# Optimization experiments

Measured on AMD Instinct MI355X. Metric: run time of the kernel, lower is better.

## Reference

```python
import jax, jax.numpy as jnp
import numpy as np

B, N, D = 16, 2048, 1024
H, DH = 8, 64
I = H * DH            # 512
L = 64                # num_latents
DEPTH = 6
FF = 4 * D


def setup_inputs() -> dict:
    key = jax.random.key(0)
    ks = jax.random.split(key, 8)
    s = 0.02  # weight scale to keep activations well-conditioned
    return {
        "x": jax.random.normal(ks[0], (B, N, D), jnp.float32),
        "mask": jax.random.randint(ks[1], (B, N), 0, 2, jnp.int32),
        "latents": jax.random.normal(ks[2], (L, D), jnp.float32),
        "ln_m_w": jnp.ones((DEPTH, D), jnp.float32),
        "ln_m_b": jnp.zeros((DEPTH, D), jnp.float32),
        "ln_l_w": jnp.ones((DEPTH, D), jnp.float32),
        "ln_l_b": jnp.zeros((DEPTH, D), jnp.float32),
        "Wq": jax.random.normal(ks[3], (DEPTH, D, I), jnp.float32) * s,
        "Wkv": jax.random.normal(ks[4], (DEPTH, D, 2 * I), jnp.float32) * s,
        "Wo": jax.random.normal(ks[5], (DEPTH, I, D), jnp.float32) * s,
        "ff_ln_w": jnp.ones((DEPTH, D), jnp.float32),
        "ff_ln_b": jnp.zeros((DEPTH, D), jnp.float32),
        "W1": jax.random.normal(ks[6], (DEPTH, D, FF), jnp.float32) * s,
        "W2": jax.random.normal(ks[7], (DEPTH, FF, D), jnp.float32) * s,
        "norm_w": jnp.ones((D,), jnp.float32),
        "norm_b": jnp.zeros((D,), jnp.float32),
    }


def _ln(x, w, b, eps=1e-5):
    mu = x.mean(-1, keepdims=True)
    var = ((x - mu) ** 2).mean(-1, keepdims=True)
    return (x - mu) * jax.lax.rsqrt(var + eps) * w + b


def reference(x, mask, latents, ln_m_w, ln_m_b, ln_l_w, ln_l_b,
              Wq, Wkv, Wo, ff_ln_w, ff_ln_b, W1, W2, norm_w, norm_b):
    b, n, d = x.shape
    Lq = latents.shape[0]
    depth = Wq.shape[0]
    h = H
    dh = Wq.shape[-1] // h
    scale = dh ** -0.5

    x4 = x[:, None]  # b 1 n d  (t = 1 media frame)
    lat = jnp.broadcast_to(latents, (b, 1, Lq, d)).astype(x.dtype)
    # mask==1 means masked-out; latents (L zeros) are always attendable
    fmask = jnp.concatenate([mask, jnp.zeros((b, Lq), mask.dtype)], axis=-1)
    mbool = (fmask == 1)[:, None, None, None, :]  # b 1 1 1 S -> broadcast to b t h i S

    for i in range(depth):
        xn = _ln(x4, ln_m_w[i], ln_m_b[i])
        lnl = _ln(lat, ln_l_w[i], ln_l_b[i])
        q = (lnl @ Wq[i]).reshape(b, 1, Lq, h, dh)
        kv = jnp.concatenate([xn, lnl], axis=-2) @ Wkv[i]  # b 1 S 2I
        k, v = jnp.split(kv, 2, axis=-1)
        S = k.shape[-2]
        k = k.reshape(b, 1, S, h, dh)
        v = v.reshape(b, 1, S, h, dh)
        sim = jnp.einsum('btihd,btjhd->bthij', q, k) * scale
        sim = jnp.where(mbool, -jnp.inf, sim)
        sim = sim - jax.lax.stop_gradient(sim.max(axis=-1, keepdims=True))
        attn = jax.nn.softmax(sim, axis=-1)
        out = jnp.einsum('bthij,btjhd->btihd', attn, v).reshape(b, 1, Lq, h * dh)
        lat = out @ Wo[i] + lat
        hf = jax.nn.gelu(_ln(lat, ff_ln_w[i], ff_ln_b[i]) @ W1[i], approximate=False)
        lat = hf @ W2[i] + lat
    return _ln(lat, norm_w, norm_b)
```

## Files before the change

### kernel.cpp

```cpp
#include <hip/hip_runtime.h>

typedef unsigned short u16;
typedef unsigned int u32;
typedef __attribute__((ext_vector_type(8))) short short8;
typedef __attribute__((ext_vector_type(4))) float f4;

#define DEV static __device__ __forceinline__

constexpr int BB = 16, NN = 2048, DD = 1024, HH = 8, DHD = 64, II = 512, LL = 64, DEPTHC = 6, FFC = 4096;

DEV u16 f2bf(float f) {
  union { float f; u32 u; } v; v.f = f;
  u32 r = v.u + 0x7FFFu + ((v.u >> 16) & 1u);
  return (u16)(r >> 16);
}

typedef const u32 __attribute__((address_space(1)))* gas_p;
typedef u32 __attribute__((address_space(3)))* las_p;
DEV void gl_lds16(const void* g, void* l) {
  __builtin_amdgcn_global_load_lds((gas_p)g, (las_p)l, 16, 0, 0);
}

__global__ __launch_bounds__(256) void maskscan_k(const int* __restrict__ mask,
    int* __restrict__ idx, int* __restrict__ cnt) {
  int b = blockIdx.x, tid = threadIdx.x;
  int lane = tid & 63, wv = tid >> 6;
  const int* mrow = mask + (size_t)b * NN;
  int base = tid * 8;
  int keep[8]; int local = 0;
  #pragma unroll
  for (int j = 0; j < 8; j++) { keep[j] = (mrow[base + j] == 0); local += keep[j]; }
  int incl = local;
  #pragma unroll
  for (int off = 1; off < 64; off <<= 1) {
    int v = __shfl_up(incl, off, 64);
    if (lane >= off) incl += v;
  }
  __shared__ int wsum[4];
  if (lane == 63) wsum[wv] = incl;
  __syncthreads();
  int wbase = 0;
  for (int w = 0; w < wv; w++) wbase += wsum[w];
  int pos = wbase + incl - local;
  #pragma unroll
  for (int j = 0; j < 8; j++) if (keep[j]) idx[(size_t)b * NN + pos++] = base + j;
  if (tid == 255) cnt[b] = wbase + incl;
}

__global__ __launch_bounds__(256) void ln_gather_k(const float* __restrict__ x,
    const int* __restrict__ idx, const int* __restrict__ cnt, u16* __restrict__ xcomp) {
  int b = blockIdx.y, j = blockIdx.x, tid = threadIdx.x;
  int c = cnt[b];
  if (j >= ((c + 127) & ~127)) return;
  ushort4* orow = (ushort4*)(xcomp + ((size_t)b * NN + j) * DD);
  if (j >= c) { orow[tid] = make_ushort4(0, 0, 0, 0); return; }
  int src = idx[(size_t)b * NN + j];
  const float4* rp = (const float4*)(x + ((size_t)b * NN + src) * DD);
  float4 v = rp[tid];
  float s = v.x + v.y + v.z + v.w;
  float s2 = v.x*v.x + v.y*v.y + v.z*v.z + v.w*v.w;
  #pragma unroll
  for (int off = 32; off >= 1; off >>= 1) {
    s  += __shfl_xor(s, off, 64);
    s2 += __shfl_xor(s2, off, 64);
  }
  __shared__ float red[8];
  int wv = tid >> 6;
  if ((tid & 63) == 0) { red[wv] = s; red[4 + wv] = s2; }
  __syncthreads();
  s  = red[0] + red[1] + red[2] + red[3];
  s2 = red[4] + red[5] + red[6] + red[7];
  float mu = s * (1.f / DD);
  float var = s2 * (1.f / DD) - mu * mu;
  float rstd = rsqrtf(var + 1e-5f);
  orow[tid] = make_ushort4(f2bf((v.x - mu) * rstd), f2bf((v.y - mu) * rstd),
                           f2bf((v.z - mu) * rstd), f2bf((v.w - mu) * rstd));
}

template<bool OUTF32>
__global__ __launch_bounds__(256) void ln_rows_k(const float* __restrict__ in,
    const float* __restrict__ w, const float* __restrict__ bias, void* __restrict__ out) {
  int row = blockIdx.x;
  int tid = threadIdx.x;
  const float4* rp = (const float4*)(in + (size_t)row * DD);
  float4 x = rp[tid];
  float s = x.x + x.y + x.z + x.w;
  float s2 = x.x*x.x + x.y*x.y + x.z*x.z + x.w*x.w;
  #pragma unroll
  for (int off = 32; off >= 1; off >>= 1) {
    s  += __shfl_xor(s, off, 64);
    s2 += __shfl_xor(s2, off, 64);
  }
  __shared__ float red[8];
  int wv = tid >> 6;
  if ((tid & 63) == 0) { red[wv] = s; red[4 + wv] = s2; }
  __syncthreads();
  s  = red[0] + red[1] + red[2] + red[3];
  s2 = red[4] + red[5] + red[6] + red[7];
  float mu = s * (1.f / DD);
  float var = s2 * (1.f / DD) - mu * mu;
  float rstd = rsqrtf(var + 1e-5f);
  float y[4] = {x.x, x.y, x.z, x.w};
  int col = tid * 4;
  #pragma unroll
  for (int j = 0; j < 4; j++)
    y[j] = (y[j] - mu) * rstd * w[col + j] + bias[col + j];
  if (OUTF32) {
    float4 o = {y[0], y[1], y[2], y[3]};
    ((float4*)out)[(size_t)row * (DD/4) + tid] = o;
  } else {
    ushort4 o = make_ushort4(f2bf(y[0]), f2bf(y[1]), f2bf(y[2]), f2bf(y[3]));
    ((ushort4*)out)[(size_t)row * (DD/4) + tid] = o;
  }
}

__global__ __launch_bounds__(256) void lat_init_k(const float* __restrict__ latents, float* __restrict__ lat) {
  int idx = blockIdx.x * 256 + threadIdx.x;
  ((float4*)lat)[idx] = ((const float4*)latents)[idx & (LL * DD / 4 - 1)];
}

__global__ void zero_k(float* __restrict__ p, int n) {
  int i = blockIdx.x * 256 + threadIdx.x;
  if (i < n) p[i] = 0.f;
}

__global__ void transpall_k(const float* __restrict__ WqA, const float* __restrict__ WkvA,
    const float* __restrict__ WoA, const float* __restrict__ W1A, const float* __restrict__ W2A,
    const float* __restrict__ lnwA, const float* __restrict__ lnbA,
    u16* __restrict__ WqkvTA, u16* __restrict__ WkvTfA, u16* __restrict__ WoTA,
    u16* __restrict__ W1TA, u16* __restrict__ W2TA, float* __restrict__ biaskvA) {
  __shared__ float t[32][33];
  __shared__ float bred[8][32];
  int gid = blockIdx.x;
  int depth = gid / 10240;
  int id = gid % 10240;
  const float* in; u16* o1; int R, C, c0, r0;
  bool iskv = false;
  if (id < 512)       { in = WqA  + (size_t)depth*1024*512;  R = 1024; C = 512;  int l = id;        c0 = (l % 16) * 32;  r0 = (l / 16) * 32;  o1 = WqkvTA + (size_t)depth*1536*1024; }
  else if (id < 1536) { in = WkvA + (size_t)depth*1024*1024; R = 1024; C = 1024; int l = id - 512;  c0 = (l % 32) * 32;  r0 = (l / 32) * 32;  o1 = WqkvTA + (size_t)depth*1536*1024 + 512*1024; iskv = true; }
  else if (id < 2048) { in = WoA  + (size_t)depth*512*1024;  R = 512;  C = 1024; int l = id - 1536; c0 = (l % 32) * 32;  r0 = (l / 32) * 32;  o1 = WoTA + (size_t)depth*1024*512; }
  else if (id < 6144) { in = W1A  + (size_t)depth*1024*4096; R = 1024; C = 4096; int l = id - 2048; c0 = (l % 128) * 32; r0 = (l / 128) * 32; o1 = W1TA + (size_t)depth*4096*1024; }
  else                { in = W2A  + (size_t)depth*4096*1024; R = 4096; C = 1024; int l = id - 6144; c0 = (l % 32) * 32;  r0 = (l / 32) * 32;  o1 = W2TA + (size_t)depth*1024*4096; }
  int tx = threadIdx.x, ty = threadIdx.y;
  #pragma unroll
  for (int j = 0; j < 4; j++)
    t[ty + j*8][tx] = in[(size_t)(r0 + ty + j*8) * C + c0 + tx];
  __syncthreads();
  #pragma unroll
  for (int j = 0; j < 4; j++)
    o1[(size_t)(c0 + ty + j*8) * R + r0 + tx] = f2bf(t[tx][ty + j*8]);
  if (iskv) {
    const float* lnw = lnwA + depth * 1024;
    const float* lnb = lnbA + depth * 1024;
    u16* WkvTf = WkvTfA + (size_t)depth*1024*1024;
    float sc = lnw[r0 + tx];
    #pragma unroll
    for (int j = 0; j < 4; j++)
      WkvTf[(size_t)(c0 + ty + j*8) * 1024 + r0 + tx] = f2bf(t[tx][ty + j*8] * sc);
    float partial = 0.f;
    #pragma unroll
    for (int rr = 0; rr < 4; rr++)
      partial += lnb[r0 + ty + rr*8] * t[ty + rr*8][tx];
    bred[ty][tx] = partial;
    __syncthreads();
    if (ty == 0) {
      float sum = 0.f;
      #pragma unroll
      for (int w = 0; w < 8; w++) sum += bred[w][tx];
      atomicAdd(&biaskvA[depth*1024 + c0 + tx], sum);
    }
  }
}

__global__ __launch_bounds__(256) void gemm_fused_k(
    const u16* __restrict__ xcomp, const u16* __restrict__ WkvTf, u16* __restrict__ kvx,
    const float* __restrict__ bias, const int* __restrict__ cnt,
    const u16* __restrict__ lnl, const u16* __restrict__ WqkvT, u16* __restrict__ qkv) {
  __shared__ __align__(16) u16 As[128 * 32];
  __shared__ __align__(16) u16 Bs[128 * 32];
  int id = blockIdx.x;
  int tid = threadIdx.x;
  int wv = tid >> 6, lane = tid & 63;
  const u16 *A, *B; u16* C; int N; bool dobias;
  int m0, n0;
  if (id < 2048) {
    int xg = id & 7, t = id >> 3;
    int mtile = xg * 32 + (t >> 3);
    n0 = (t & 7) * 128;
    int batch = mtile >> 4;
    int ml = (mtile & 15) * 128;
    if (ml >= cnt[batch]) return;
    m0 = batch * NN + ml;
    A = xcomp; B = WkvTf; C = kvx; N = 1024; dobias = true;
  } else {
    int l = id - 2048;
    m0 = (l / 12) * 128; n0 = (l % 12) * 128;
    A = lnl; B = WqkvT; C = qkv; N = 1536; dobias = false;
  }
  const int K = 1024;
  int srow = wv * 16 + (lane >> 2);
  int scol = (lane & 3) * 8;
  const u16* gA0 = A + (size_t)(m0 + srow) * K + scol;
  const u16* gA1 = A + (size_t)(m0 + 64 + srow) * K + scol;
  const u16* gB0 = B + (size_t)(n0 + srow) * K + scol;
  const u16* gB1 = B + (size_t)(n0 + 64 + srow) * K + scol;
  u16* lA0 = &As[srow * 32 + scol];
  u16* lA1 = &As[(64 + srow) * 32 + scol];
  u16* lB0 = &Bs[srow * 32 + scol];
  u16* lB1 = &Bs[(64 + srow) * 32 + scol];
  int wm = (wv & 1) * 64, wn = (wv >> 1) * 64;
  int fr = lane & 15, fq = (lane >> 4) * 8;
  f4 acc[4][4];
  #pragma unroll
  for (int mi = 0; mi < 4; mi++)
    #pragma unroll
    for (int ni = 0; ni < 4; ni++) acc[mi][ni] = f4{0.f, 0.f, 0.f, 0.f};

  for (int k0 = 0; k0 < K; k0 += 32) {
    gl_lds16(gA0 + k0, lA0);
    gl_lds16(gA1 + k0, lA1);
    gl_lds16(gB0 + k0, lB0);
    gl_lds16(gB1 + k0, lB1);
    __syncthreads();
    short8 af[4], bfr[4];
    #pragma unroll
    for (int mi = 0; mi < 4; mi++)
      af[mi] = *(const short8*)&As[(wm + mi*16 + fr) * 32 + fq];
    #pragma unroll
    for (int ni = 0; ni < 4; ni++)
      bfr[ni] = *(const short8*)&Bs[(wn + ni*16 + fr) * 32 + fq];
    #pragma unroll
    for (int mi = 0; mi < 4; mi++)
      #pragma unroll
      for (int ni = 0; ni < 4; ni++)
        acc[mi][ni] = __builtin_amdgcn_mfma_f32_16x16x32_bf16(af[mi], bfr[ni], acc[mi][ni], 0, 0, 0);
    __syncthreads();
  }
  int er = (lane >> 4) * 4;
  int ec = lane & 15;
  #pragma unroll
  for (int mi = 0; mi < 4; mi++) {
    #pragma unroll
    for (int ni = 0; ni < 4; ni++) {
      int col = n0 + wn + ni*16 + ec;
      float bv = dobias ? bias[col] : 0.f;
      #pragma unroll
      for (int r = 0; r < 4; r++) {
        int row = m0 + wm + mi*16 + er + r;
        C[(size_t)row * N + col] = f2bf(acc[mi][ni][r] + bv);
      }
    }
  }
}

__global__ __launch_bounds__(256) void gemm_gelu_k(const u16* __restrict__ A, const u16* __restrict__ Bm,
    u16* __restrict__ C, int M, int N, int K) {
  __shared__ __align__(16) u16 As[128 * 32];
  __shared__ __align__(16) u16 Bs[128 * 32];
  int tid = threadIdx.x;
  int wv = tid >> 6, lane = tid & 63;
  int m0 = blockIdx.y * 128, n0 = blockIdx.x * 128;
  int srow = wv * 16 + (lane >> 2);
  int scol = (lane & 3) * 8;
  const u16* gA0 = A + (size_t)(m0 + srow) * K + scol;
  const u16* gA1 = A + (size_t)(m0 + 64 + srow) * K + scol;
  const u16* gB0 = Bm + (size_t)(n0 + srow) * K + scol;
  const u16* gB1 = Bm + (size_t)(n0 + 64 + srow) * K + scol;
  u16* lA0 = &As[srow * 32 + scol];
  u16* lA1 = &As[(64 + srow) * 32 + scol];
  u16* lB0 = &Bs[srow * 32 + scol];
  u16* lB1 = &Bs[(64 + srow) * 32 + scol];
  int wm = (wv & 1) * 64, wn = (wv >> 1) * 64;
  int fr = lane & 15, fq = (lane >> 4) * 8;
  f4 acc[4][4];
  #pragma unroll
  for (int mi = 0; mi < 4; mi++)
    #pragma unroll
    for (int ni = 0; ni < 4; ni++) acc[mi][ni] = f4{0.f, 0.f, 0.f, 0.f};

  for (int k0 = 0; k0 < K; k0 += 32) {
    gl_lds16(gA0 + k0, lA0);
    gl_lds16(gA1 + k0, lA1);
    gl_lds16(gB0 + k0, lB0);
    gl_lds16(gB1 + k0, lB1);
    __syncthreads();
    short8 af[4], bfr[4];
    #pragma unroll
    for (int mi = 0; mi < 4; mi++)
      af[mi] = *(const short8*)&As[(wm + mi*16 + fr) * 32 + fq];
    #pragma unroll
    for (int ni = 0; ni < 4; ni++)
      bfr[ni] = *(const short8*)&Bs[(wn + ni*16 + fr) * 32 + fq];
    #pragma unroll
    for (int mi = 0; mi < 4; mi++)
      #pragma unroll
      for (int ni = 0; ni < 4; ni++)
        acc[mi][ni] = __builtin_amdgcn_mfma_f32_16x16x32_bf16(af[mi], bfr[ni], acc[mi][ni], 0, 0, 0);
    __syncthreads();
  }
  int er = (lane >> 4) * 4;
  int ec = lane & 15;
  #pragma unroll
  for (int mi = 0; mi < 4; mi++)
    #pragma unroll
    for (int ni = 0; ni < 4; ni++) {
      int col = n0 + wn + ni*16 + ec;
      #pragma unroll
      for (int r = 0; r < 4; r++) {
        int row = m0 + wm + mi*16 + er + r;
        float v = acc[mi][ni][r];
        v = 0.5f * v * (1.f + erff(v * 0.70710678118654752f));
        C[(size_t)row * N + col] = f2bf(v);
      }
    }
}

__global__ __launch_bounds__(256) void gemmsk_k(const u16* __restrict__ A, const u16* __restrict__ Bm,
    float* __restrict__ C, int M, int N, int K, int Kc) {
  __shared__ __align__(16) u16 As[128 * 32];
  __shared__ __align__(16) u16 Bs[128 * 32];
  int tid = threadIdx.x;
  int wv = tid >> 6, lane = tid & 63;
  int m0 = blockIdx.y * 128, n0 = blockIdx.x * 128;
  int kb = blockIdx.z * Kc;
  int srow = wv * 16 + (lane >> 2);
  int scol = (lane & 3) * 8;
  const u16* gA0 = A + (size_t)(m0 + srow) * K + kb + scol;
  const u16* gA1 = A + (size_t)(m0 + 64 + srow) * K + kb + scol;
  const u16* gB0 = Bm + (size_t)(n0 + srow) * K + kb + scol;
  const u16* gB1 = Bm + (size_t)(n0 + 64 + srow) * K + kb + scol;
  u16* lA0 = &As[srow * 32 + scol];
  u16* lA1 = &As[(64 + srow) * 32 + scol];
  u16* lB0 = &Bs[srow * 32 + scol];
  u16* lB1 = &Bs[(64 + srow) * 32 + scol];
  int wm = (wv & 1) * 64, wn = (wv >> 1) * 64;
  int fr = lane & 15, fq = (lane >> 4) * 8;
  f4 acc[4][4];
  #pragma unroll
  for (int mi = 0; mi < 4; mi++)
    #pragma unroll
    for (int ni = 0; ni < 4; ni++) acc[mi][ni] = f4{0.f, 0.f, 0.f, 0.f};

  for (int k0 = 0; k0 < Kc; k0 += 32) {
    gl_lds16(gA0 + k0, lA0);
    gl_lds16(gA1 + k0, lA1);
    gl_lds16(gB0 + k0, lB0);
    gl_lds16(gB1 + k0, lB1);
    __syncthreads();
    short8 af[4], bfr[4];
    #pragma unroll
    for (int mi = 0; mi < 4; mi++)
      af[mi] = *(const short8*)&As[(wm + mi*16 + fr) * 32 + fq];
    #pragma unroll
    for (int ni = 0; ni < 4; ni++)
      bfr[ni] = *(const short8*)&Bs[(wn + ni*16 + fr) * 32 + fq];
    #pragma unroll
    for (int mi = 0; mi < 4; mi++)
      #pragma unroll
      for (int ni = 0; ni < 4; ni++)
        acc[mi][ni] = __builtin_amdgcn_mfma_f32_16x16x32_bf16(af[mi], bfr[ni], acc[mi][ni], 0, 0, 0);
    __syncthreads();
  }
  int er = (lane >> 4) * 4;
  int ec = lane & 15;
  #pragma unroll
  for (int mi = 0; mi < 4; mi++)
    #pragma unroll
    for (int ni = 0; ni < 4; ni++) {
      int col = n0 + wn + ni*16 + ec;
      #pragma unroll
      for (int r = 0; r < 4; r++) {
        int row = m0 + wm + mi*16 + er + r;
        atomicAdd(&C[(size_t)row * N + col], acc[mi][ni][r]);
      }
    }
}

__global__ __launch_bounds__(256) void attn_part_k(const u16* __restrict__ qkv,
    const u16* __restrict__ kvx, const int* __restrict__ cnt,
    float* __restrict__ opart, float* __restrict__ mlpart) {
  int id = blockIdx.x;
  int b = id >> 4;
  int h = (id >> 1) & 7;
  int half = id & 1;
  int tid = threadIdx.x;
  int wv = tid >> 6, lane = tid & 63;
  int fr = lane & 15, fq8 = (lane >> 4) * 8;
  int c = cnt[b];
  int nt = (c + 63) >> 6;
  int T = nt + 1;
  int t0 = half ? (T >> 1) : 0;
  int t1 = half ? T : (T >> 1);

  __shared__ __align__(16) u16 ks[64 * 88];
  __shared__ __align__(16) u16 vs[64 * 88];
  __shared__ __align__(16) u16 ps[4][16 * 88];
  __shared__ float smask[64];

  const u16* qp = qkv + (size_t)(b * LL + wv * 16 + fr) * 1536 + h * DHD;
  short8 aq0 = *(const short8*)(qp + fq8);
  short8 aq1 = *(const short8*)(qp + 32 + fq8);

  float m_i[4], l_i[4];
  f4 o[4];
  #pragma unroll
  for (int r = 0; r < 4; r++) { m_i[r] = -1e30f; l_i[r] = 0.f; }
  #pragma unroll
  for (int dt = 0; dt < 4; dt++) o[dt] = f4{0.f, 0.f, 0.f, 0.f};

  const float scale = 0.125f;

  for (int t = t0; t < t1; t++) {
    bool isLat = (t == nt);
    const u16* src;
    int rs;
    if (isLat) { src = qkv + (size_t)(b * LL) * 1536 + 512 + h * DHD; rs = 1536; }
    else       { src = kvx + (size_t)(b * NN + t * 64) * 1024 + h * DHD; rs = 1024; }
    __syncthreads();
    #pragma unroll
    for (int it = 0; it < 2; it++) {
      int cid = it * 256 + tid;
      int kr = cid >> 3, c8 = (cid & 7) * 8;
      int4 kvv = *(const int4*)(src + (size_t)kr * rs + c8);
      *(int4*)&ks[kr * 88 + c8] = kvv;
      int4 vvv = *(const int4*)(src + 512 + (size_t)kr * rs + c8);
      const u16* ve = (const u16*)&vvv;
      #pragma unroll
      for (int j = 0; j < 8; j++) vs[(c8 + j) * 88 + kr] = ve[j];
    }
    if (tid < 64)
      smask[tid] = (isLat || (t * 64 + tid < c)) ? 0.f : -1e30f;
    __syncthreads();

    f4 sim[4];
    #pragma unroll
    for (int ct = 0; ct < 4; ct++) {
      short8 b0 = *(const short8*)&ks[(ct*16 + fr) * 88 + fq8];
      short8 b1 = *(const short8*)&ks[(ct*16 + fr) * 88 + 32 + fq8];
      f4 s = f4{0.f, 0.f, 0.f, 0.f};
      s = __builtin_amdgcn_mfma_f32_16x16x32_bf16(aq0, b0, s, 0, 0, 0);
      s = __builtin_amdgcn_mfma_f32_16x16x32_bf16(aq1, b1, s, 0, 0, 0);
      float mk = smask[ct*16 + fr];
      #pragma unroll
      for (int r = 0; r < 4; r++) s[r] = s[r] * scale + mk;
      sim[ct] = s;
    }
    float mnew[4], alpha[4], p[4][4];
    #pragma unroll
    for (int r = 0; r < 4; r++) {
      float mx = fmaxf(fmaxf(sim[0][r], sim[1][r]), fmaxf(sim[2][r], sim[3][r]));
      #pragma unroll
      for (int off = 8; off >= 1; off >>= 1) mx = fmaxf(mx, __shfl_xor(mx, off, 16));
      mnew[r] = fmaxf(m_i[r], mx);
      alpha[r] = __expf(m_i[r] - mnew[r]);
      m_i[r] = mnew[r];
      float ssum = 0.f;
      #pragma unroll
      for (int ct = 0; ct < 4; ct++) { float e = __expf(sim[ct][r] - mnew[r]); p[ct][r] = e; ssum += e; }
      #pragma unroll
      for (int off = 8; off >= 1; off >>= 1) ssum += __shfl_xor(ssum, off, 16);
      l_i[r] = l_i[r] * alpha[r] + ssum;
    }
    #pragma unroll
    for (int ct = 0; ct < 4; ct++)
      #pragma unroll
      for (int r = 0; r < 4; r++)
        ps[wv][((lane>>4)*4 + r) * 88 + ct*16 + fr] = f2bf(p[ct][r]);
    #pragma unroll
    for (int dt = 0; dt < 4; dt++)
      #pragma unroll
      for (int r = 0; r < 4; r++) o[dt][r] *= alpha[r];
    short8 pa0 = *(const short8*)&ps[wv][fr * 88 + fq8];
    short8 pa1 = *(const short8*)&ps[wv][fr * 88 + 32 + fq8];
    #pragma unroll
    for (int dt = 0; dt < 4; dt++) {
      short8 bv0 = *(const short8*)&vs[(dt*16 + fr) * 88 + fq8];
      short8 bv1 = *(const short8*)&vs[(dt*16 + fr) * 88 + 32 + fq8];
      o[dt] = __builtin_amdgcn_mfma_f32_16x16x32_bf16(pa0, bv0, o[dt], 0, 0, 0);
      o[dt] = __builtin_amdgcn_mfma_f32_16x16x32_bf16(pa1, bv1, o[dt], 0, 0, 0);
    }
  }
  #pragma unroll
  for (int dt = 0; dt < 4; dt++)
    #pragma unroll
    for (int r = 0; r < 4; r++) {
      int row = wv * 16 + (lane>>4)*4 + r;
      int col = dt*16 + fr;
      opart[((size_t)id * 64 + row) * 64 + col] = o[dt][r];
    }
  if (fr == 0) {
    #pragma unroll
    for (int r = 0; r < 4; r++) {
      int row = wv * 16 + (lane>>4)*4 + r;
      mlpart[id * 128 + row * 2]     = m_i[r];
      mlpart[id * 128 + row * 2 + 1] = l_i[r];
    }
  }
}

__global__ __launch_bounds__(256) void attn_comb_k(const float* __restrict__ opart,
    const float* __restrict__ mlpart, u16* __restrict__ out) {
  int bh = blockIdx.x;
  int b = bh >> 3, h = bh & 7;
  int id0 = bh * 2, id1 = bh * 2 + 1;
  int tid = threadIdx.x;
  int row = tid >> 2;
  int c0 = (tid & 3) * 16;
  float m0 = mlpart[id0 * 128 + row * 2], l0 = mlpart[id0 * 128 + row * 2 + 1];
  float m1 = mlpart[id1 * 128 + row * 2], l1 = mlpart[id1 * 128 + row * 2 + 1];
  float m = fmaxf(m0, m1);
  float a0 = __expf(m0 - m), a1 = __expf(m1 - m);
  float rl = 1.f / (l0 * a0 + l1 * a1);
  const float4* p0 = (const float4*)(opart + ((size_t)id0 * 64 + row) * 64 + c0);
  const float4* p1 = (const float4*)(opart + ((size_t)id1 * 64 + row) * 64 + c0);
  u16* op = out + ((size_t)(b * LL + row)) * II + h * DHD + c0;
  #pragma unroll
  for (int j = 0; j < 4; j++) {
    float4 v0 = p0[j], v1 = p1[j];
    op[j*4 + 0] = f2bf((v0.x * a0 + v1.x * a1) * rl);
    op[j*4 + 1] = f2bf((v0.y * a0 + v1.y * a1) * rl);
    op[j*4 + 2] = f2bf((v0.z * a0 + v1.z * a1) * rl);
    op[j*4 + 3] = f2bf((v0.w * a0 + v1.w * a1) * rl);
  }
}

extern "C" void kernel_launch(void* const* d_in, const int* in_sizes, int n_in,
                              void* d_out, int out_size, void* d_ws, size_t ws_size,
                              hipStream_t stream) {
  (void)in_sizes; (void)n_in; (void)out_size; (void)ws_size;
  const float* x       = (const float*)d_in[0];
  const int*   mask    = (const int*)d_in[1];
  const float* latents = (const float*)d_in[2];
  const float* ln_m_w  = (const float*)d_in[3];
  const float* ln_m_b  = (const float*)d_in[4];
  const float* ln_l_w  = (const float*)d_in[5];
  const float* ln_l_b  = (const float*)d_in[6];
  const float* Wq      = (const float*)d_in[7];
  const float* Wkv     = (const float*)d_in[8];
  const float* Wo      = (const float*)d_in[9];
  const float* ff_ln_w = (const float*)d_in[10];
  const float* ff_ln_b = (const float*)d_in[11];
  const float* W1      = (const float*)d_in[12];
  const float* W2      = (const float*)d_in[13];
  const float* norm_w  = (const float*)d_in[14];
  const float* norm_b  = (const float*)d_in[15];
  float* out = (float*)d_out;

  char* ws = (char*)d_ws;
  size_t off = 0;
  auto alloc = [&](size_t bytes) -> void* {
    void* p = ws + off; off += (bytes + 255) & ~(size_t)255; return p;
  };
  u16* xcomp = (u16*)alloc((size_t)32768 * 1024 * 2);
  u16* kvx   = (u16*)alloc((size_t)32768 * 1024 * 2);
  int* idxb  = (int*)alloc((size_t)32768 * 4);
  int* cnt   = (int*)alloc(64);
  float* lat = (float*)alloc((size_t)1024 * 1024 * 4);
  u16* lnl   = (u16*)alloc((size_t)1024 * 1024 * 2);
  u16* latn  = (u16*)alloc((size_t)1024 * 1024 * 2);
  u16* qkv   = (u16*)alloc((size_t)1024 * 1536 * 2);
  u16* aout  = (u16*)alloc((size_t)1024 * 512 * 2);
  u16* hf    = (u16*)alloc((size_t)1024 * 4096 * 2);
  float* opart  = (float*)alloc((size_t)256 * 64 * 64 * 4);
  float* mlpart = (float*)alloc((size_t)256 * 128 * 4);
  u16* WqkvT = (u16*)alloc((size_t)DEPTHC * 1536 * 1024 * 2);
  u16* WkvTf = (u16*)alloc((size_t)DEPTHC * 1024 * 1024 * 2);
  u16* WoT   = (u16*)alloc((size_t)DEPTHC * 1024 * 512 * 2);
  u16* W1T   = (u16*)alloc((size_t)DEPTHC * 4096 * 1024 * 2);
  u16* W2T   = (u16*)alloc((size_t)DEPTHC * 1024 * 4096 * 2);
  float* biaskv_all = (float*)alloc(DEPTHC * 1024 * 4);

  maskscan_k<<<16, 256, 0, stream>>>(mask, idxb, cnt);
  ln_gather_k<<<dim3(2048, 16), 256, 0, stream>>>(x, idxb, cnt, xcomp);
  lat_init_k<<<1024, 256, 0, stream>>>(latents, lat);
  zero_k<<<24, 256, 0, stream>>>(biaskv_all, DEPTHC * 1024);
  transpall_k<<<DEPTHC * 10240, dim3(32, 8), 0, stream>>>(
      Wq, Wkv, Wo, W1, W2, ln_m_w, ln_m_b,
      WqkvT, WkvTf, WoT, W1T, W2T, biaskv_all);

  for (int i = 0; i < DEPTHC; i++) {
    ln_rows_k<false><<<1024, 256, 0, stream>>>(lat, ln_l_w + i*1024, ln_l_b + i*1024, lnl);
    gemm_fused_k<<<2144, 256, 0, stream>>>(
        xcomp, WkvTf + (size_t)i*1024*1024, kvx, biaskv_all + i*1024, cnt,
        lnl, WqkvT + (size_t)i*1536*1024, qkv);
    attn_part_k<<<256, 256, 0, stream>>>(qkv, kvx, cnt, opart, mlpart);
    attn_comb_k<<<128, 256, 0, stream>>>(opart, mlpart, aout);
    gemmsk_k<<<dim3(8, 8, 4), 256, 0, stream>>>(aout, WoT + (size_t)i*1024*512, lat, 1024, 1024, 512, 128);
    ln_rows_k<false><<<1024, 256, 0, stream>>>(lat, ff_ln_w + i*1024, ff_ln_b + i*1024, latn);
    gemm_gelu_k<<<dim3(32, 8), 256, 0, stream>>>(latn, W1T + (size_t)i*4096*1024, hf, 1024, 4096, 1024);
    gemmsk_k<<<dim3(8, 8, 4), 256, 0, stream>>>(hf, W2T + (size_t)i*1024*4096, lat, 1024, 1024, 4096, 1024);
  }
  ln_rows_k<true><<<1024, 256, 0, stream>>>(lat, norm_w, norm_b, out);
}
```

Baseline: 1.497 ms.

## Fuse layernorms into GEMMs, merge setup kernels, transpose V layout

Folds the latent and feed-forward layernorm affine parameters into pre-transposed weights plus precomputed bias vectors. The per-row normalization now runs inside the QKV and W1 GEMM prologues, so the separate ln_rows launches go away. The attention-combine step is merged into the Wo GEMM, and the small setup kernels are merged into one launch. The transpose kernel moves to 64x64 tiles with 16-byte packed stores, and K/V are written split with V transposed, so the attention kernel no longer scatters V into LDS. The cost is more work per GEMM block: redundant row statistics and a float-to-bf16 conversion on the A-tile path.

```diff
diff --git a/kernel.cpp b/kernel.cpp
--- a/kernel.cpp
+++ b/kernel.cpp
@@ -15,36 +15,54 @@
   return (u16)(r >> 16);
 }
 
+DEV void pack8(const float* v, u16* dst) {
+  union { u16 u[8]; int4 i; } p;
+  #pragma unroll
+  for (int e = 0; e < 8; e++) p.u[e] = f2bf(v[e]);
+  *(int4*)dst = p.i;
+}
+
 typedef const u32 __attribute__((address_space(1)))* gas_p;
 typedef u32 __attribute__((address_space(3)))* las_p;
 DEV void gl_lds16(const void* g, void* l) {
   __builtin_amdgcn_global_load_lds((gas_p)g, (las_p)l, 16, 0, 0);
 }
 
-__global__ __launch_bounds__(256) void maskscan_k(const int* __restrict__ mask,
-    int* __restrict__ idx, int* __restrict__ cnt) {
-  int b = blockIdx.x, tid = threadIdx.x;
-  int lane = tid & 63, wv = tid >> 6;
-  const int* mrow = mask + (size_t)b * NN;
-  int base = tid * 8;
-  int keep[8]; int local = 0;
-  #pragma unroll
-  for (int j = 0; j < 8; j++) { keep[j] = (mrow[base + j] == 0); local += keep[j]; }
-  int incl = local;
-  #pragma unroll
-  for (int off = 1; off < 64; off <<= 1) {
-    int v = __shfl_up(incl, off, 64);
-    if (lane >= off) incl += v;
-  }
-  __shared__ int wsum[4];
-  if (lane == 63) wsum[wv] = incl;
-  __syncthreads();
-  int wbase = 0;
-  for (int w = 0; w < wv; w++) wbase += wsum[w];
-  int pos = wbase + incl - local;
-  #pragma unroll
-  for (int j = 0; j < 8; j++) if (keep[j]) idx[(size_t)b * NN + pos++] = base + j;
-  if (tid == 255) cnt[b] = wbase + incl;
+__global__ __launch_bounds__(256) void pre0_k(const int* __restrict__ mask,
+    int* __restrict__ idx, int* __restrict__ cnt,
+    const float* __restrict__ latents, float* __restrict__ lat,
+    float* __restrict__ biasall, int nbias) {
+  int bid = blockIdx.x, tid = threadIdx.x;
+  if (bid < 16) {
+    int b = bid;
+    int lane = tid & 63, wv = tid >> 6;
+    const int* mrow = mask + (size_t)b * NN;
+    int base = tid * 8;
+    int keep[8]; int local = 0;
+    #pragma unroll
+    for (int j = 0; j < 8; j++) { keep[j] = (mrow[base + j] == 0); local += keep[j]; }
+    int incl = local;
+    #pragma unroll
+    for (int off = 1; off < 64; off <<= 1) {
+      int v = __shfl_up(incl, off, 64);
+      if (lane >= off) incl += v;
+    }
+    __shared__ int wsum[4];
+    if (lane == 63) wsum[wv] = incl;
+    __syncthreads();
+    int wbase = 0;
+    for (int w = 0; w < wv; w++) wbase += wsum[w];
+    int pos = wbase + incl - local;
+    #pragma unroll
+    for (int j = 0; j < 8; j++) if (keep[j]) idx[(size_t)b * NN + pos++] = base + j;
+    if (tid == 255) cnt[b] = wbase + incl;
+  } else if (bid < 16 + 1024) {
+    int i = (bid - 16) * 256 + tid;
+    ((float4*)lat)[i] = ((const float4*)latents)[i & (LL * DD / 4 - 1)];
+  } else {
+    int i = ((bid - 1040) * 256 + tid) * 4;
+    if (i < nbias) *(float4*)(biasall + i) = float4{0.f, 0.f, 0.f, 0.f};
+  }
 }
 
 __global__ __launch_bounds__(256) void ln_gather_k(const float* __restrict__ x,
@@ -77,9 +95,8 @@
                            f2bf((v.z - mu) * rstd), f2bf((v.w - mu) * rstd));
 }
 
-template<bool OUTF32>
-__global__ __launch_bounds__(256) void ln_rows_k(const float* __restrict__ in,
-    const float* __restrict__ w, const float* __restrict__ bias, void* __restrict__ out) {
+__global__ __launch_bounds__(256) void ln_final_k(const float* __restrict__ in,
+    const float* __restrict__ w, const float* __restrict__ bias, float* __restrict__ out) {
   int row = blockIdx.x;
   int tid = threadIdx.x;
   const float4* rp = (const float4*)(in + (size_t)row * DD);
@@ -100,112 +117,423 @@
   float mu = s * (1.f / DD);
   float var = s2 * (1.f / DD) - mu * mu;
   float rstd = rsqrtf(var + 1e-5f);
-  float y[4] = {x.x, x.y, x.z, x.w};
   int col = tid * 4;
-  #pragma unroll
-  for (int j = 0; j < 4; j++)
-    y[j] = (y[j] - mu) * rstd * w[col + j] + bias[col + j];
-  if (OUTF32) {
-    float4 o = {y[0], y[1], y[2], y[3]};
-    ((float4*)out)[(size_t)row * (DD/4) + tid] = o;
+  float4 o;
+  o.x = (x.x - mu) * rstd * w[col+0] + bias[col+0];
+  o.y = (x.y - mu) * rstd * w[col+1] + bias[col+1];
+  o.z = (x.z - mu) * rstd * w[col+2] + bias[col+2];
+  o.w = (x.w - mu) * rstd * w[col+3] + bias[col+3];
+  ((float4*)out)[(size_t)row * (DD/4) + tid] = o;
+}
+
+__global__ __launch_bounds__(256) void transpall_k(const float* __restrict__ WqA,
+    const float* __restrict__ WkvA, const float* __restrict__ WoA,
+    const float* __restrict__ W1A, const float* __restrict__ W2A,
+    const float* __restrict__ lnlw, const float* __restrict__ lnlb,
+    const float* __restrict__ lnmw, const float* __restrict__ lnmb,
+    const float* __restrict__ ffw, const float* __restrict__ ffb,
+    u16* __restrict__ WqkvTA, u16* __restrict__ WkvTfA, u16* __restrict__ WoTA,
+    u16* __restrict__ W1TA, u16* __restrict__ W2TA, float* __restrict__ biasall) {
+  __shared__ float t[64][67];
+  __shared__ float sw1[64], sw2[64], sb1[64], sb2[64];
+  __shared__ float bred[64][4];
+  int gid = blockIdx.x, tid = threadIdx.x;
+  int depth = gid / 2560;
+  int id = gid % 2560;
+  float* biasqkv = biasall + depth * 1536;
+  float* biaskv  = biasall + DEPTHC*1536 + depth * 1024;
+  float* bias1   = biasall + DEPTHC*1536 + DEPTHC*1024 + depth * 4096;
+  const float* in; int R, C, c0, r0;
+  u16 *o1, *o2 = nullptr;
+  const float *w1v = nullptr, *w2v = nullptr, *b1v = nullptr, *b2v = nullptr;
+  float *bo1 = nullptr, *bo2 = nullptr;
+  if (id < 128) {
+    in = WqA + (size_t)depth*1024*512; R = 1024; C = 512;
+    r0 = (id >> 3) * 64; c0 = (id & 7) * 64;
+    o1 = WqkvTA + (size_t)depth*1536*1024;
+    w1v = lnlw + depth*1024; b1v = lnlb + depth*1024; bo1 = biasqkv;
+  } else if (id < 384) {
+    int l = id - 128;
+    in = WkvA + (size_t)depth*1024*1024; R = 1024; C = 1024;
+    r0 = (l >> 4) * 64; c0 = (l & 15) * 64;
+    o1 = WqkvTA + (size_t)depth*1536*1024 + (size_t)512*1024;
+    w1v = lnlw + depth*1024; b1v = lnlb + depth*1024; bo1 = biasqkv + 512;
+    o2 = WkvTfA + (size_t)depth*1024*1024;
+    w2v = lnmw + depth*1024; b2v = lnmb + depth*1024; bo2 = biaskv;
+  } else if (id < 512) {
+    int l = id - 384;
+    in = WoA + (size_t)depth*512*1024; R = 512; C = 1024;
+    r0 = (l >> 4) * 64; c0 = (l & 15) * 64;
+    o1 = WoTA + (size_t)depth*1024*512;
+  } else if (id < 1536) {
+    int l = id - 512;
+    in = W1A + (size_t)depth*1024*4096; R = 1024; C = 4096;
+    r0 = (l >> 6) * 64; c0 = (l & 63) * 64;
+    o1 = W1TA + (size_t)depth*4096*1024;
+    w1v = ffw + depth*1024; b1v = ffb + depth*1024; bo1 = bias1;
   } else {
-    ushort4 o = make_ushort4(f2bf(y[0]), f2bf(y[1]), f2bf(y[2]), f2bf(y[3]));
-    ((ushort4*)out)[(size_t)row * (DD/4) + tid] = o;
-  }
-}
-
-__global__ __launch_bounds__(256) void lat_init_k(const float* __restrict__ latents, float* __restrict__ lat) {
-  int idx = blockIdx.x * 256 + threadIdx.x;
-  ((float4*)lat)[idx] = ((const float4*)latents)[idx & (LL * DD / 4 - 1)];
-}
-
-__global__ void zero_k(float* __restrict__ p, int n) {
-  int i = blockIdx.x * 256 + threadIdx.x;
-  if (i < n) p[i] = 0.f;
-}
-
-__global__ void transpall_k(const float* __restrict__ WqA, const float* __restrict__ WkvA,
-    const float* __restrict__ WoA, const float* __restrict__ W1A, const float* __restrict__ W2A,
-    const float* __restrict__ lnwA, const float* __restrict__ lnbA,
-    u16* __restrict__ WqkvTA, u16* __restrict__ WkvTfA, u16* __restrict__ WoTA,
-    u16* __restrict__ W1TA, u16* __restrict__ W2TA, float* __restrict__ biaskvA) {
-  __shared__ float t[32][33];
-  __shared__ float bred[8][32];
-  int gid = blockIdx.x;
-  int depth = gid / 10240;
-  int id = gid % 10240;
-  const float* in; u16* o1; int R, C, c0, r0;
-  bool iskv = false;
-  if (id < 512)       { in = WqA  + (size_t)depth*1024*512;  R = 1024; C = 512;  int l = id;        c0 = (l % 16) * 32;  r0 = (l / 16) * 32;  o1 = WqkvTA + (size_t)depth*1536*1024; }
-  else if (id < 1536) { in = WkvA + (size_t)depth*1024*1024; R = 1024; C = 1024; int l = id - 512;  c0 = (l % 32) * 32;  r0 = (l / 32) * 32;  o1 = WqkvTA + (size_t)depth*1536*1024 + 512*1024; iskv = true; }
-  else if (id < 2048) { in = WoA  + (size_t)depth*512*1024;  R = 512;  C = 1024; int l = id - 1536; c0 = (l % 32) * 32;  r0 = (l / 32) * 32;  o1 = WoTA + (size_t)depth*1024*512; }
-  else if (id < 6144) { in = W1A  + (size_t)depth*1024*4096; R = 1024; C = 4096; int l = id - 2048; c0 = (l % 128) * 32; r0 = (l / 128) * 32; o1 = W1TA + (size_t)depth*4096*1024; }
-  else                { in = W2A  + (size_t)depth*4096*1024; R = 4096; C = 1024; int l = id - 6144; c0 = (l % 32) * 32;  r0 = (l / 32) * 32;  o1 = W2TA + (size_t)depth*1024*4096; }
-  int tx = threadIdx.x, ty = threadIdx.y;
-  #pragma unroll
-  for (int j = 0; j < 4; j++)
-    t[ty + j*8][tx] = in[(size_t)(r0 + ty + j*8) * C + c0 + tx];
+    int l = id - 1536;
+    in = W2A + (size_t)depth*4096*1024; R = 4096; C = 1024;
+    r0 = (l >> 4) * 64; c0 = (l & 15) * 64;
+    o1 = W2TA + (size_t)depth*1024*4096;
+  }
+  #pragma unroll
+  for (int j = 0; j < 4; j++) {
+    int rr = (tid >> 4) + j * 16;
+    float4 v = *(const float4*)(in + (size_t)(r0 + rr) * C + c0 + (tid & 15) * 4);
+    int cc = (tid & 15) * 4;
+    t[rr][cc+0] = v.x; t[rr][cc+1] = v.y; t[rr][cc+2] = v.z; t[rr][cc+3] = v.w;
+  }
+  if (tid < 64) {
+    sw1[tid] = w1v ? w1v[r0 + tid] : 1.f;
+    sb1[tid] = b1v ? b1v[r0 + tid] : 0.f;
+    sw2[tid] = w2v ? w2v[r0 + tid] : 1.f;
+    sb2[tid] = b2v ? b2v[r0 + tid] : 0.f;
+  }
   __syncthreads();
   #pragma unroll
-  for (int j = 0; j < 4; j++)
-    o1[(size_t)(c0 + ty + j*8) * R + r0 + tx] = f2bf(t[tx][ty + j*8]);
-  if (iskv) {
-    const float* lnw = lnwA + depth * 1024;
-    const float* lnb = lnbA + depth * 1024;
-    u16* WkvTf = WkvTfA + (size_t)depth*1024*1024;
-    float sc = lnw[r0 + tx];
-    #pragma unroll
-    for (int j = 0; j < 4; j++)
-      WkvTf[(size_t)(c0 + ty + j*8) * 1024 + r0 + tx] = f2bf(t[tx][ty + j*8] * sc);
-    float partial = 0.f;
-    #pragma unroll
-    for (int rr = 0; rr < 4; rr++)
-      partial += lnb[r0 + ty + rr*8] * t[ty + rr*8][tx];
-    bred[ty][tx] = partial;
-    __syncthreads();
-    if (ty == 0) {
-      float sum = 0.f;
-      #pragma unroll
-      for (int w = 0; w < 8; w++) sum += bred[w][tx];
-      atomicAdd(&biaskvA[depth*1024 + c0 + tx], sum);
-    }
+  for (int p = 0; p < 2; p++) {
+    int ch = p * 256 + tid;
+    int oc = ch >> 3;
+    int or8 = (ch & 7) * 8;
+    float v[8], vv[8];
+    #pragma unroll
+    for (int e = 0; e < 8; e++) v[e] = t[or8 + e][oc];
+    #pragma unroll
+    for (int e = 0; e < 8; e++) vv[e] = v[e] * sw1[or8 + e];
+    pack8(vv, o1 + (size_t)(c0 + oc) * R + r0 + or8);
+    if (o2) {
+      #pragma unroll
+      for (int e = 0; e < 8; e++) vv[e] = v[e] * sw2[or8 + e];
+      pack8(vv, o2 + (size_t)(c0 + oc) * R + r0 + or8);
+    }
+  }
+  if (bo1) {
+    int c = tid >> 2, q = tid & 3;
+    float a = 0.f;
+    #pragma unroll
+    for (int i = 0; i < 16; i++) a += sb1[q*16 + i] * t[q*16 + i][c];
+    bred[c][q] = a;
+    __syncthreads();
+    if (tid < 64) atomicAdd(&bo1[c0 + tid], bred[tid][0] + bred[tid][1] + bred[tid][2] + bred[tid][3]);
+  }
+  if (bo2) {
+    __syncthreads();
+    int c = tid >> 2, q = tid & 3;
+    float a = 0.f;
+    #pragma unroll
+    for (int i = 0; i < 16; i++) a += sb2[q*16 + i] * t[q*16 + i][c];
+    bred[c][q] = a;
+    __syncthreads();
+    if (tid < 64) atomicAdd(&bo2[c0 + tid], bred[tid][0] + bred[tid][1] + bred[tid][2] + bred[tid][3]);
   }
 }
 
 __global__ __launch_bounds__(256) void gemm_fused_k(
-    const u16* __restrict__ xcomp, const u16* __restrict__ WkvTf, u16* __restrict__ kvx,
-    const float* __restrict__ bias, const int* __restrict__ cnt,
-    const u16* __restrict__ lnl, const u16* __restrict__ WqkvT, u16* __restrict__ qkv) {
+    const u16* __restrict__ xcomp, const u16* __restrict__ WkvTf, const float* __restrict__ biaskv,
+    u16* __restrict__ kx, u16* __restrict__ vxT, const int* __restrict__ cnt,
+    const float* __restrict__ lat, const u16* __restrict__ WqkvT, const float* __restrict__ biasqkv,
+    u16* __restrict__ qk, u16* __restrict__ vlatT) {
   __shared__ __align__(16) u16 As[128 * 32];
   __shared__ __align__(16) u16 Bs[128 * 32];
-  int id = blockIdx.x;
-  int tid = threadIdx.x;
+  __shared__ float smu[128], srs[128];
+  int id = blockIdx.x, tid = threadIdx.x;
   int wv = tid >> 6, lane = tid & 63;
-  const u16 *A, *B; u16* C; int N; bool dobias;
-  int m0, n0;
+  int srow = wv * 16 + (lane >> 2);
+  int scol = (lane & 3) * 8;
+  int wm = (wv & 1) * 64, wn = (wv >> 1) * 64;
+  int fr = lane & 15, fq = (lane >> 4) * 8;
+  f4 acc[4][4];
+  #pragma unroll
+  for (int mi = 0; mi < 4; mi++)
+    #pragma unroll
+    for (int ni = 0; ni < 4; ni++) acc[mi][ni] = f4{0.f, 0.f, 0.f, 0.f};
+  int er = (lane >> 4) * 4;
+  int ec = lane & 15;
+
   if (id < 2048) {
     int xg = id & 7, t = id >> 3;
     int mtile = xg * 32 + (t >> 3);
-    n0 = (t & 7) * 128;
+    int n0 = (t & 7) * 128;
     int batch = mtile >> 4;
     int ml = (mtile & 15) * 128;
     if (ml >= cnt[batch]) return;
-    m0 = batch * NN + ml;
-    A = xcomp; B = WkvTf; C = kvx; N = 1024; dobias = true;
+    size_t arow = (size_t)batch * NN + ml;
+    const u16* gA0 = xcomp + (arow + srow) * 1024 + scol;
+    const u16* gA1 = xcomp + (arow + 64 + srow) * 1024 + scol;
+    const u16* gB0 = WkvTf + (size_t)(n0 + srow) * 1024 + scol;
+    const u16* gB1 = WkvTf + (size_t)(n0 + 64 + srow) * 1024 + scol;
+    u16* lA0 = &As[srow * 32 + scol];
+    u16* lA1 = &As[(64 + srow) * 32 + scol];
+    u16* lB0 = &Bs[srow * 32 + scol];
+    u16* lB1 = &Bs[(64 + srow) * 32 + scol];
+    for (int k0 = 0; k0 < 1024; k0 += 32) {
+      gl_lds16(gA0 + k0, lA0);
+      gl_lds16(gA1 + k0, lA1);
+      gl_lds16(gB0 + k0, lB0);
+      gl_lds16(gB1 + k0, lB1);
+      __syncthreads();
+      short8 af[4], bfr[4];
+      #pragma unroll
+      for (int mi = 0; mi < 4; mi++) af[mi] = *(const short8*)&As[(wm + mi*16 + fr) * 32 + fq];
+      #pragma unroll
+      for (int ni = 0; ni < 4; ni++) bfr[ni] = *(const short8*)&Bs[(wn + ni*16 + fr) * 32 + fq];
+      #pragma unroll
+      for (int mi = 0; mi < 4; mi++)
+        #pragma unroll
+        for (int ni = 0; ni < 4; ni++)
+          acc[mi][ni] = __builtin_amdgcn_mfma_f32_16x16x32_bf16(af[mi], bfr[ni], acc[mi][ni], 0, 0, 0);
+      __syncthreads();
+    }
+    #pragma unroll
+    for (int mi = 0; mi < 4; mi++) {
+      #pragma unroll
+      for (int ni = 0; ni < 4; ni++) {
+        int col = n0 + wn + ni*16 + ec;
+        float bv = biaskv[col];
+        int rbase = ml + wm + mi*16 + er;
+        if (col < 512) {
+          #pragma unroll
+          for (int r = 0; r < 4; r++)
+            kx[((size_t)batch * NN + rbase + r) * 512 + col] = f2bf(acc[mi][ni][r] + bv);
+        } else {
+          union { u16 u[4]; ushort4 s; } pk;
+          #pragma unroll
+          for (int r = 0; r < 4; r++) pk.u[r] = f2bf(acc[mi][ni][r] + bv);
+          *(ushort4*)&vxT[((size_t)batch * 512 + (col - 512)) * NN + rbase] = pk.s;
+        }
+      }
+    }
   } else {
     int l = id - 2048;
-    m0 = (l / 12) * 128; n0 = (l % 12) * 128;
-    A = lnl; B = WqkvT; C = qkv; N = 1536; dobias = false;
-  }
-  const int K = 1024;
+    int m0 = (l / 12) * 128, n0 = (l % 12) * 128;
+    for (int rr = 0; rr < 32; rr++) {
+      int row = m0 + wv * 32 + rr;
+      const float4* rp = (const float4*)(lat + (size_t)row * 1024);
+      float s = 0.f, s2 = 0.f;
+      #pragma unroll
+      for (int it = 0; it < 4; it++) {
+        float4 v = rp[it * 64 + lane];
+        s += v.x + v.y + v.z + v.w;
+        s2 += v.x*v.x + v.y*v.y + v.z*v.z + v.w*v.w;
+      }
+      #pragma unroll
+      for (int off = 32; off >= 1; off >>= 1) {
+        s  += __shfl_xor(s, off, 64);
+        s2 += __shfl_xor(s2, off, 64);
+      }
+      if (lane == 0) {
+        float mu = s * (1.f/1024.f);
+        float var = s2 * (1.f/1024.f) - mu * mu;
+        smu[wv*32 + rr] = mu;
+        srs[wv*32 + rr] = rsqrtf(var + 1e-5f);
+      }
+    }
+    __syncthreads();
+    const u16* gB0 = WqkvT + (size_t)(n0 + srow) * 1024 + scol;
+    const u16* gB1 = WqkvT + (size_t)(n0 + 64 + srow) * 1024 + scol;
+    u16* lB0 = &Bs[srow * 32 + scol];
+    u16* lB1 = &Bs[(64 + srow) * 32 + scol];
+    for (int k0 = 0; k0 < 1024; k0 += 32) {
+      #pragma unroll
+      for (int cc = 0; cc < 2; cc++) {
+        int ch = tid * 2 + cc;
+        int row = ch >> 2, c8 = (ch & 3) * 8;
+        const float4* lp = (const float4*)(lat + (size_t)(m0 + row) * 1024 + k0 + c8);
+        float4 a = lp[0], b = lp[1];
+        float mu = smu[row], rs = srs[row];
+        float v[8] = {(a.x-mu)*rs, (a.y-mu)*rs, (a.z-mu)*rs, (a.w-mu)*rs,
+                      (b.x-mu)*rs, (b.y-mu)*rs, (b.z-mu)*rs, (b.w-mu)*rs};
+        pack8(v, &As[row * 32 + c8]);
+      }
+      gl_lds16(gB0 + k0, lB0);
+      gl_lds16(gB1 + k0, lB1);
+      __syncthreads();
+      short8 af[4], bfr[4];
+      #pragma unroll
+      for (int mi = 0; mi < 4; mi++) af[mi] = *(const short8*)&As[(wm + mi*16 + fr) * 32 + fq];
+      #pragma unroll
+      for (int ni = 0; ni < 4; ni++) bfr[ni] = *(const short8*)&Bs[(wn + ni*16 + fr) * 32 + fq];
+      #pragma unroll
+      for (int mi = 0; mi < 4; mi++)
+        #pragma unroll
+        for (int ni = 0; ni < 4; ni++)
+          acc[mi][ni] = __builtin_amdgcn_mfma_f32_16x16x32_bf16(af[mi], bfr[ni], acc[mi][ni], 0, 0, 0);
+      __syncthreads();
+    }
+    #pragma unroll
+    for (int mi = 0; mi < 4; mi++) {
+      #pragma unroll
+      for (int ni = 0; ni < 4; ni++) {
+        int col = n0 + wn + ni*16 + ec;
+        float bv = biasqkv[col];
+        int rbase = m0 + wm + mi*16 + er;
+        if (col < 1024) {
+          #pragma unroll
+          for (int r = 0; r < 4; r++)
+            qk[(size_t)(rbase + r) * 1024 + col] = f2bf(acc[mi][ni][r] + bv);
+        } else {
+          int b = rbase >> 6, qrow = rbase & 63;
+          union { u16 u[4]; ushort4 s; } pk;
+          #pragma unroll
+          for (int r = 0; r < 4; r++) pk.u[r] = f2bf(acc[mi][ni][r] + bv);
+          *(ushort4*)&vlatT[((size_t)b * 512 + (col - 1024)) * 64 + qrow] = pk.s;
+        }
+      }
+    }
+  }
+}
+
+__global__ __launch_bounds__(256) void attn_part_k(const u16* __restrict__ qk,
+    const u16* __restrict__ vlatT, const u16* __restrict__ kx, const u16* __restrict__ vxT,
+    const int* __restrict__ cnt, float* __restrict__ opart, float* __restrict__ mlpart) {
+  int id = blockIdx.x;
+  int b = id >> 4;
+  int h = (id >> 1) & 7;
+  int half = id & 1;
+  int tid = threadIdx.x;
+  int wv = tid >> 6, lane = tid & 63;
+  int fr = lane & 15, fq8 = (lane >> 4) * 8;
+  int c = cnt[b];
+  int nt = (c + 63) >> 6;
+  int T = nt + 1;
+  int t0 = half ? (T >> 1) : 0;
+  int t1 = half ? T : (T >> 1);
+
+  __shared__ __align__(16) u16 ks[64 * 72];
+  __shared__ __align__(16) u16 vs[64 * 72];
+  __shared__ __align__(16) u16 ps[4][16 * 72];
+  __shared__ float smask[64];
+
+  const u16* qp = qk + (size_t)(b * LL + wv * 16 + fr) * 1024 + h * DHD;
+  short8 aq0 = *(const short8*)(qp + fq8);
+  short8 aq1 = *(const short8*)(qp + 32 + fq8);
+
+  float m_i[4], l_i[4];
+  f4 o[4];
+  #pragma unroll
+  for (int r = 0; r < 4; r++) { m_i[r] = -1e30f; l_i[r] = 0.f; }
+  #pragma unroll
+  for (int dt = 0; dt < 4; dt++) o[dt] = f4{0.f, 0.f, 0.f, 0.f};
+
+  const float scale = 0.125f;
+
+  for (int t = t0; t < t1; t++) {
+    bool isLat = (t == nt);
+    const u16 *srck, *srcv;
+    int strk, strv;
+    if (isLat) {
+      srck = qk + (size_t)(b * LL) * 1024 + 512 + h * DHD; strk = 1024;
+      srcv = vlatT + (size_t)(b * 512 + h * DHD) * 64;     strv = 64;
+    } else {
+      srck = kx + ((size_t)b * NN + t * 64) * 512 + h * DHD; strk = 512;
+      srcv = vxT + ((size_t)b * 512 + h * DHD) * NN + t * 64; strv = NN;
+    }
+    __syncthreads();
+    #pragma unroll
+    for (int it = 0; it < 2; it++) {
+      int cid = it * 256 + tid;
+      int kr = cid >> 3, c8 = (cid & 7) * 8;
+      *(int4*)&ks[kr * 72 + c8] = *(const int4*)(srck + (size_t)kr * strk + c8);
+      *(int4*)&vs[kr * 72 + c8] = *(const int4*)(srcv + (size_t)kr * strv + c8);
+    }
+    if (tid < 64)
+      smask[tid] = (isLat || (t * 64 + tid < c)) ? 0.f : -1e30f;
+    __syncthreads();
+
+    f4 sim[4];
+    #pragma unroll
+    for (int ct = 0; ct < 4; ct++) {
+      short8 b0 = *(const short8*)&ks[(ct*16 + fr) * 72 + fq8];
+      short8 b1 = *(const short8*)&ks[(ct*16 + fr) * 72 + 32 + fq8];
+      f4 s = f4{0.f, 0.f, 0.f, 0.f};
+      s = __builtin_amdgcn_mfma_f32_16x16x32_bf16(aq0, b0, s, 0, 0, 0);
+      s = __builtin_amdgcn_mfma_f32_16x16x32_bf16(aq1, b1, s, 0, 0, 0);
+      float mk = smask[ct*16 + fr];
+      #pragma unroll
+      for (int r = 0; r < 4; r++) s[r] = s[r] * scale + mk;
+      sim[ct] = s;
+    }
+    float mnew[4], alpha[4], p[4][4];
+    #pragma unroll
+    for (int r = 0; r < 4; r++) {
+      float mx = fmaxf(fmaxf(sim[0][r], sim[1][r]), fmaxf(sim[2][r], sim[3][r]));
+      #pragma unroll
+      for (int off = 8; off >= 1; off >>= 1) mx = fmaxf(mx, __shfl_xor(mx, off, 16));
+      mnew[r] = fmaxf(m_i[r], mx);
+      alpha[r] = __expf(m_i[r] - mnew[r]);
+      m_i[r] = mnew[r];
+      float ssum = 0.f;
+      #pragma unroll
+      for (int ct = 0; ct < 4; ct++) { float e = __expf(sim[ct][r] - mnew[r]); p[ct][r] = e; ssum += e; }
+      #pragma unroll
+      for (int off = 8; off >= 1; off >>= 1) ssum += __shfl_xor(ssum, off, 16);
+      l_i[r] = l_i[r] * alpha[r] + ssum;
+    }
+    #pragma unroll
+    for (int ct = 0; ct < 4; ct++)
+      #pragma unroll
+      for (int r = 0; r < 4; r++)
+        ps[wv][((lane>>4)*4 + r) * 72 + ct*16 + fr] = f2bf(p[ct][r]);
+    #pragma unroll
+    for (int dt = 0; dt < 4; dt++)
+      #pragma unroll
+      for (int r = 0; r < 4; r++) o[dt][r] *= alpha[r];
+    short8 pa0 = *(const short8*)&ps[wv][fr * 72 + fq8];
+    short8 pa1 = *(const short8*)&ps[wv][fr * 72 + 32 + fq8];
+    #pragma unroll
+    for (int dt = 0; dt < 4; dt++) {
+      short8 bv0 = *(const short8*)&vs[(dt*16 + fr) * 72 + fq8];
+      short8 bv1 = *(const short8*)&vs[(dt*16 + fr) * 72 + 32 + fq8];
+      o[dt] = __builtin_amdgcn_mfma_f32_16x16x32_bf16(pa0, bv0, o[dt], 0, 0, 0);
+      o[dt] = __builtin_amdgcn_mfma_f32_16x16x32_bf16(pa1, bv1, o[dt], 0, 0, 0);
+    }
+  }
+  #pragma unroll
+  for (int dt = 0; dt < 4; dt++)
+    #pragma unroll
+    for (int r = 0; r < 4; r++) {
+      int row = wv * 16 + (lane>>4)*4 + r;
+      int col = dt*16 + fr;
+      opart[((size_t)id * 64 + row) * 64 + col] = o[dt][r];
+    }
+  if (fr == 0) {
+    #pragma unroll
+    for (int r = 0; r < 4; r++) {
+      int row = wv * 16 + (lane>>4)*4 + r;
+      mlpart[id * 128 + row * 2]     = m_i[r];
+      mlpart[id * 128 + row * 2 + 1] = l_i[r];
+    }
+  }
+}
+
+__global__ __launch_bounds__(256) void gemm_wo_k(const float* __restrict__ opart,
+    const float* __restrict__ mlpart, const u16* __restrict__ WoT, float* __restrict__ lat) {
+  __shared__ __align__(16) u16 As[128 * 32];
+  __shared__ __align__(16) u16 Bs[128 * 32];
+  __shared__ float f0s[128][2], f1s[128][2];
+  int tid = threadIdx.x;
+  int wv = tid >> 6, lane = tid & 63;
+  int m0 = blockIdx.y * 128, n0 = blockIdx.x * 128, kb = blockIdx.z * 128;
+  int h0 = kb >> 6;
+  {
+    int row = tid >> 1, hh = tid & 1;
+    int grow = m0 + row;
+    int gb = grow >> 6, qrow = grow & 63;
+    int id0 = (gb * 8 + h0 + hh) * 2;
+    float ma = mlpart[id0 * 128 + qrow * 2],       la = mlpart[id0 * 128 + qrow * 2 + 1];
+    float mb = mlpart[(id0 + 1) * 128 + qrow * 2], lb = mlpart[(id0 + 1) * 128 + qrow * 2 + 1];
+    float mm = fmaxf(ma, mb);
+    float a0 = __expf(ma - mm), a1 = __expf(mb - mm);
+    float rl = 1.f / (la * a0 + lb * a1);
+    f0s[row][hh] = a0 * rl;
+    f1s[row][hh] = a1 * rl;
+  }
+  __syncthreads();
   int srow = wv * 16 + (lane >> 2);
   int scol = (lane & 3) * 8;
-  const u16* gA0 = A + (size_t)(m0 + srow) * K + scol;
-  const u16* gA1 = A + (size_t)(m0 + 64 + srow) * K + scol;
-  const u16* gB0 = B + (size_t)(n0 + srow) * K + scol;
-  const u16* gB1 = B + (size_t)(n0 + 64 + srow) * K + scol;
-  u16* lA0 = &As[srow * 32 + scol];
-  u16* lA1 = &As[(64 + srow) * 32 + scol];
+  const u16* gB0 = WoT + (size_t)(n0 + srow) * 512 + kb + scol;
+  const u16* gB1 = WoT + (size_t)(n0 + 64 + srow) * 512 + kb + scol;
   u16* lB0 = &Bs[srow * 32 + scol];
   u16* lB1 = &Bs[(64 + srow) * 32 + scol];
   int wm = (wv & 1) * 64, wn = (wv >> 1) * 64;
@@ -216,19 +544,34 @@
     #pragma unroll
     for (int ni = 0; ni < 4; ni++) acc[mi][ni] = f4{0.f, 0.f, 0.f, 0.f};
 
-  for (int k0 = 0; k0 < K; k0 += 32) {
-    gl_lds16(gA0 + k0, lA0);
-    gl_lds16(gA1 + k0, lA1);
-    gl_lds16(gB0 + k0, lB0);
-    gl_lds16(gB1 + k0, lB1);
+  for (int ki = 0; ki < 4; ki++) {
+    int k0 = kb + ki * 32;
+    #pragma unroll
+    for (int cc = 0; cc < 2; cc++) {
+      int ch = tid * 2 + cc;
+      int row = ch >> 2, c8 = (ch & 3) * 8;
+      int koff = k0 + c8;
+      int hh = (koff - kb) >> 6;
+      int kc = koff & 63;
+      int grow = m0 + row;
+      int gb = grow >> 6, qrow = grow & 63;
+      int id0 = (gb * 8 + h0 + hh) * 2;
+      const float4* p0 = (const float4*)(opart + ((size_t)id0 * 64 + qrow) * 64 + kc);
+      const float4* p1 = (const float4*)(opart + ((size_t)(id0 + 1) * 64 + qrow) * 64 + kc);
+      float4 x0 = p0[0], x1 = p0[1], y0 = p1[0], y1 = p1[1];
+      float f0 = f0s[row][hh], f1 = f1s[row][hh];
+      float v[8] = {x0.x*f0 + y0.x*f1, x0.y*f0 + y0.y*f1, x0.z*f0 + y0.z*f1, x0.w*f0 + y0.w*f1,
+                    x1.x*f0 + y1.x*f1, x1.y*f0 + y1.y*f1, x1.z*f0 + y1.z*f1, x1.w*f0 + y1.w*f1};
+      pack8(v, &As[row * 32 + c8]);
+    }
+    gl_lds16(gB0 + ki * 32, lB0);
+    gl_lds16(gB1 + ki * 32, lB1);
     __syncthreads();
     short8 af[4], bfr[4];
     #pragma unroll
-    for (int mi = 0; mi < 4; mi++)
-      af[mi] = *(const short8*)&As[(wm + mi*16 + fr) * 32 + fq];
-    #pragma unroll
-    for (int ni = 0; ni < 4; ni++)
-      bfr[ni] = *(const short8*)&Bs[(wn + ni*16 + fr) * 32 + fq];
+    for (int mi = 0; mi < 4; mi++) af[mi] = *(const short8*)&As[(wm + mi*16 + fr) * 32 + fq];
+    #pragma unroll
+    for (int ni = 0; ni < 4; ni++) bfr[ni] = *(const short8*)&Bs[(wn + ni*16 + fr) * 32 + fq];
     #pragma unroll
     for (int mi = 0; mi < 4; mi++)
       #pragma unroll
@@ -239,35 +582,53 @@
   int er = (lane >> 4) * 4;
   int ec = lane & 15;
   #pragma unroll
-  for (int mi = 0; mi < 4; mi++) {
+  for (int mi = 0; mi < 4; mi++)
     #pragma unroll
     for (int ni = 0; ni < 4; ni++) {
       int col = n0 + wn + ni*16 + ec;
-      float bv = dobias ? bias[col] : 0.f;
       #pragma unroll
       for (int r = 0; r < 4; r++) {
         int row = m0 + wm + mi*16 + er + r;
-        C[(size_t)row * N + col] = f2bf(acc[mi][ni][r] + bv);
+        atomicAdd(&lat[(size_t)row * 1024 + col], acc[mi][ni][r]);
       }
     }
-  }
-}
-
-__global__ __launch_bounds__(256) void gemm_gelu_k(const u16* __restrict__ A, const u16* __restrict__ Bm,
-    u16* __restrict__ C, int M, int N, int K) {
+}
+
+__global__ __launch_bounds__(256) void gemm_gelu_ln_k(const float* __restrict__ lat,
+    const u16* __restrict__ W1T, const float* __restrict__ bias1, u16* __restrict__ hf) {
   __shared__ __align__(16) u16 As[128 * 32];
   __shared__ __align__(16) u16 Bs[128 * 32];
+  __shared__ float smu[128], srs[128];
   int tid = threadIdx.x;
   int wv = tid >> 6, lane = tid & 63;
   int m0 = blockIdx.y * 128, n0 = blockIdx.x * 128;
+  for (int rr = 0; rr < 32; rr++) {
+    int row = m0 + wv * 32 + rr;
+    const float4* rp = (const float4*)(lat + (size_t)row * 1024);
+    float s = 0.f, s2 = 0.f;
+    #pragma unroll
+    for (int it = 0; it < 4; it++) {
+      float4 v = rp[it * 64 + lane];
+      s += v.x + v.y + v.z + v.w;
+      s2 += v.x*v.x + v.y*v.y + v.z*v.z + v.w*v.w;
+    }
+    #pragma unroll
+    for (int off = 32; off >= 1; off >>= 1) {
+      s  += __shfl_xor(s, off, 64);
+      s2 += __shfl_xor(s2, off, 64);
+    }
+    if (lane == 0) {
+      float mu = s * (1.f/1024.f);
+      float var = s2 * (1.f/1024.f) - mu * mu;
+      smu[wv*32 + rr] = mu;
+      srs[wv*32 + rr] = rsqrtf(var + 1e-5f);
+    }
+  }
+  __syncthreads();
   int srow = wv * 16 + (lane >> 2);
   int scol = (lane & 3) * 8;
-  const u16* gA0 = A + (size_t)(m0 + srow) * K + scol;
-  const u16* gA1 = A + (size_t)(m0 + 64 + srow) * K + scol;
-  const u16* gB0 = Bm + (size_t)(n0 + srow) * K + scol;
-  const u16* gB1 = Bm + (size_t)(n0 + 64 + srow) * K + scol;
-  u16* lA0 = &As[srow * 32 + scol];
-  u16* lA1 = &As[(64 + srow) * 32 + scol];
+  const u16* gB0 = W1T + (size_t)(n0 + srow) * 1024 + scol;
+  const u16* gB1 = W1T + (size_t)(n0 + 64 + srow) * 1024 + scol;
   u16* lB0 = &Bs[srow * 32 + scol];
   u16* lB1 = &Bs[(64 + srow) * 32 + scol];
   int wm = (wv & 1) * 64, wn = (wv >> 1) * 64;
@@ -278,19 +639,26 @@
     #pragma unroll
     for (int ni = 0; ni < 4; ni++) acc[mi][ni] = f4{0.f, 0.f, 0.f, 0.f};
 
-  for (int k0 = 0; k0 < K; k0 += 32) {
-    gl_lds16(gA0 + k0, lA0);
-    gl_lds16(gA1 + k0, lA1);
+  for (int k0 = 0; k0 < 1024; k0 += 32) {
+    #pragma unroll
+    for (int cc = 0; cc < 2; cc++) {
+      int ch = tid * 2 + cc;
+      int row = ch >> 2, c8 = (ch & 3) * 8;
+      const float4* lp = (const float4*)(lat + (size_t)(m0 + row) * 1024 + k0 + c8);
+      float4 a = lp[0], b = lp[1];
+      float mu = smu[row], rs = srs[row];
+      float v[8] = {(a.x-mu)*rs, (a.y-mu)*rs, (a.z-mu)*rs, (a.w-mu)*rs,
+                    (b.x-mu)*rs, (b.y-mu)*rs, (b.z-mu)*rs, (b.w-mu)*rs};
+      pack8(v, &As[row * 32 + c8]);
+    }
     gl_lds16(gB0 + k0, lB0);
     gl_lds16(gB1 + k0, lB1);
     __syncthreads();
     short8 af[4], bfr[4];
     #pragma unroll
-    for (int mi = 0; mi < 4; mi++)
-      af[mi] = *(const short8*)&As[(wm + mi*16 + fr) * 32 + fq];
-    #pragma unroll
-    for (int ni = 0; ni < 4; ni++)
-      bfr[ni] = *(const short8*)&Bs[(wn + ni*16 + fr) * 32 + fq];
+    for (int mi = 0; mi < 4; mi++) af[mi] = *(const short8*)&As[(wm + mi*16 + fr) * 32 + fq];
+    #pragma unroll
+    for (int ni = 0; ni < 4; ni++) bfr[ni] = *(const short8*)&Bs[(wn + ni*16 + fr) * 32 + fq];
     #pragma unroll
     for (int mi = 0; mi < 4; mi++)
       #pragma unroll
@@ -305,12 +673,13 @@
     #pragma unroll
     for (int ni = 0; ni < 4; ni++) {
       int col = n0 + wn + ni*16 + ec;
+      float bv = bias1[col];
       #pragma unroll
       for (int r = 0; r < 4; r++) {
         int row = m0 + wm + mi*16 + er + r;
-        float v = acc[mi][ni][r];
+        float v = acc[mi][ni][r] + bv;
         v = 0.5f * v * (1.f + erff(v * 0.70710678118654752f));
-        C[(size_t)row * N + col] = f2bf(v);
+        hf[(size_t)row * 4096 + col] = f2bf(v);
       }
     }
 }
@@ -349,11 +718,9 @@
     __syncthreads();
     short8 af[4], bfr[4];
     #pragma unroll
-    for (int mi = 0; mi < 4; mi++)
-      af[mi] = *(const short8*)&As[(wm + mi*16 + fr) * 32 + fq];
-    #pragma unroll
-    for (int ni = 0; ni < 4; ni++)
-      bfr[ni] = *(const short8*)&Bs[(wn + ni*16 + fr) * 32 + fq];
+    for (int mi = 0; mi < 4; mi++) af[mi] = *(const short8*)&As[(wm + mi*16 + fr) * 32 + fq];
+    #pragma unroll
+    for (int ni = 0; ni < 4; ni++) bfr[ni] = *(const short8*)&Bs[(wn + ni*16 + fr) * 32 + fq];
     #pragma unroll
     for (int mi = 0; mi < 4; mi++)
       #pragma unroll
@@ -374,154 +741,6 @@
         atomicAdd(&C[(size_t)row * N + col], acc[mi][ni][r]);
       }
     }
-}
-
-__global__ __launch_bounds__(256) void attn_part_k(const u16* __restrict__ qkv,
-    const u16* __restrict__ kvx, const int* __restrict__ cnt,
-    float* __restrict__ opart, float* __restrict__ mlpart) {
-  int id = blockIdx.x;
-  int b = id >> 4;
-  int h = (id >> 1) & 7;
-  int half = id & 1;
-  int tid = threadIdx.x;
-  int wv = tid >> 6, lane = tid & 63;
-  int fr = lane & 15, fq8 = (lane >> 4) * 8;
-  int c = cnt[b];
-  int nt = (c + 63) >> 6;
-  int T = nt + 1;
-  int t0 = half ? (T >> 1) : 0;
-  int t1 = half ? T : (T >> 1);
-
-  __shared__ __align__(16) u16 ks[64 * 88];
-  __shared__ __align__(16) u16 vs[64 * 88];
-  __shared__ __align__(16) u16 ps[4][16 * 88];
-  __shared__ float smask[64];
-
-  const u16* qp = qkv + (size_t)(b * LL + wv * 16 + fr) * 1536 + h * DHD;
-  short8 aq0 = *(const short8*)(qp + fq8);
-  short8 aq1 = *(const short8*)(qp + 32 + fq8);
-
-  float m_i[4], l_i[4];
-  f4 o[4];
-  #pragma unroll
-  for (int r = 0; r < 4; r++) { m_i[r] = -1e30f; l_i[r] = 0.f; }
-  #pragma unroll
-  for (int dt = 0; dt < 4; dt++) o[dt] = f4{0.f, 0.f, 0.f, 0.f};
-
-  const float scale = 0.125f;
-
-  for (int t = t0; t < t1; t++) {
-    bool isLat = (t == nt);
-    const u16* src;
-    int rs;
-    if (isLat) { src = qkv + (size_t)(b * LL) * 1536 + 512 + h * DHD; rs = 1536; }
-    else       { src = kvx + (size_t)(b * NN + t * 64) * 1024 + h * DHD; rs = 1024; }
-    __syncthreads();
-    #pragma unroll
-    for (int it = 0; it < 2; it++) {
-      int cid = it * 256 + tid;
-      int kr = cid >> 3, c8 = (cid & 7) * 8;
-      int4 kvv = *(const int4*)(src + (size_t)kr * rs + c8);
-      *(int4*)&ks[kr * 88 + c8] = kvv;
-      int4 vvv = *(const int4*)(src + 512 + (size_t)kr * rs + c8);
-      const u16* ve = (const u16*)&vvv;
-      #pragma unroll
-      for (int j = 0; j < 8; j++) vs[(c8 + j) * 88 + kr] = ve[j];
-    }
-    if (tid < 64)
-      smask[tid] = (isLat || (t * 64 + tid < c)) ? 0.f : -1e30f;
-    __syncthreads();
-
-    f4 sim[4];
-    #pragma unroll
-    for (int ct = 0; ct < 4; ct++) {
-      short8 b0 = *(const short8*)&ks[(ct*16 + fr) * 88 + fq8];
-      short8 b1 = *(const short8*)&ks[(ct*16 + fr) * 88 + 32 + fq8];
-      f4 s = f4{0.f, 0.f, 0.f, 0.f};
-      s = __builtin_amdgcn_mfma_f32_16x16x32_bf16(aq0, b0, s, 0, 0, 0);
-      s = __builtin_amdgcn_mfma_f32_16x16x32_bf16(aq1, b1, s, 0, 0, 0);
-      float mk = smask[ct*16 + fr];
-      #pragma unroll
-      for (int r = 0; r < 4; r++) s[r] = s[r] * scale + mk;
-      sim[ct] = s;
-    }
-    float mnew[4], alpha[4], p[4][4];
-    #pragma unroll
-    for (int r = 0; r < 4; r++) {
-      float mx = fmaxf(fmaxf(sim[0][r], sim[1][r]), fmaxf(sim[2][r], sim[3][r]));
-      #pragma unroll
-      for (int off = 8; off >= 1; off >>= 1) mx = fmaxf(mx, __shfl_xor(mx, off, 16));
-      mnew[r] = fmaxf(m_i[r], mx);
-      alpha[r] = __expf(m_i[r] - mnew[r]);
-      m_i[r] = mnew[r];
-      float ssum = 0.f;
-      #pragma unroll
-      for (int ct = 0; ct < 4; ct++) { float e = __expf(sim[ct][r] - mnew[r]); p[ct][r] = e; ssum += e; }
-      #pragma unroll
-      for (int off = 8; off >= 1; off >>= 1) ssum += __shfl_xor(ssum, off, 16);
-      l_i[r] = l_i[r] * alpha[r] + ssum;
-    }
-    #pragma unroll
-    for (int ct = 0; ct < 4; ct++)
-      #pragma unroll
-      for (int r = 0; r < 4; r++)
-        ps[wv][((lane>>4)*4 + r) * 88 + ct*16 + fr] = f2bf(p[ct][r]);
-    #pragma unroll
-    for (int dt = 0; dt < 4; dt++)
-      #pragma unroll
-      for (int r = 0; r < 4; r++) o[dt][r] *= alpha[r];
-    short8 pa0 = *(const short8*)&ps[wv][fr * 88 + fq8];
-    short8 pa1 = *(const short8*)&ps[wv][fr * 88 + 32 + fq8];
-    #pragma unroll
-    for (int dt = 0; dt < 4; dt++) {
-      short8 bv0 = *(const short8*)&vs[(dt*16 + fr) * 88 + fq8];
-      short8 bv1 = *(const short8*)&vs[(dt*16 + fr) * 88 + 32 + fq8];
-      o[dt] = __builtin_amdgcn_mfma_f32_16x16x32_bf16(pa0, bv0, o[dt], 0, 0, 0);
-      o[dt] = __builtin_amdgcn_mfma_f32_16x16x32_bf16(pa1, bv1, o[dt], 0, 0, 0);
-    }
-  }
-  #pragma unroll
-  for (int dt = 0; dt < 4; dt++)
-    #pragma unroll
-    for (int r = 0; r < 4; r++) {
-      int row = wv * 16 + (lane>>4)*4 + r;
-      int col = dt*16 + fr;
-      opart[((size_t)id * 64 + row) * 64 + col] = o[dt][r];
-    }
-  if (fr == 0) {
-    #pragma unroll
-    for (int r = 0; r < 4; r++) {
-      int row = wv * 16 + (lane>>4)*4 + r;
-      mlpart[id * 128 + row * 2]     = m_i[r];
-      mlpart[id * 128 + row * 2 + 1] = l_i[r];
-    }
-  }
-}
-
-__global__ __launch_bounds__(256) void attn_comb_k(const float* __restrict__ opart,
-    const float* __restrict__ mlpart, u16* __restrict__ out) {
-  int bh = blockIdx.x;
-  int b = bh >> 3, h = bh & 7;
-  int id0 = bh * 2, id1 = bh * 2 + 1;
-  int tid = threadIdx.x;
-  int row = tid >> 2;
-  int c0 = (tid & 3) * 16;
-  float m0 = mlpart[id0 * 128 + row * 2], l0 = mlpart[id0 * 128 + row * 2 + 1];
-  float m1 = mlpart[id1 * 128 + row * 2], l1 = mlpart[id1 * 128 + row * 2 + 1];
-  float m = fmaxf(m0, m1);
-  float a0 = __expf(m0 - m), a1 = __expf(m1 - m);
-  float rl = 1.f / (l0 * a0 + l1 * a1);
-  const float4* p0 = (const float4*)(opart + ((size_t)id0 * 64 + row) * 64 + c0);
-  const float4* p1 = (const float4*)(opart + ((size_t)id1 * 64 + row) * 64 + c0);
-  u16* op = out + ((size_t)(b * LL + row)) * II + h * DHD + c0;
-  #pragma unroll
-  for (int j = 0; j < 4; j++) {
-    float4 v0 = p0[j], v1 = p1[j];
-    op[j*4 + 0] = f2bf((v0.x * a0 + v1.x * a1) * rl);
-    op[j*4 + 1] = f2bf((v0.y * a0 + v1.y * a1) * rl);
-    op[j*4 + 2] = f2bf((v0.z * a0 + v1.z * a1) * rl);
-    op[j*4 + 3] = f2bf((v0.w * a0 + v1.w * a1) * rl);
-  }
 }
 
 extern "C" void kernel_launch(void* const* d_in, const int* in_sizes, int n_in,
@@ -551,15 +770,14 @@
   auto alloc = [&](size_t bytes) -> void* {
     void* p = ws + off; off += (bytes + 255) & ~(size_t)255; return p;
   };
-  u16* xcomp = (u16*)alloc((size_t)32768 * 1024 * 2);
-  u16* kvx   = (u16*)alloc((size_t)32768 * 1024 * 2);
-  int* idxb  = (int*)alloc((size_t)32768 * 4);
+  u16* xcomp = (u16*)alloc((size_t)BB * NN * 1024 * 2);
+  u16* kx    = (u16*)alloc((size_t)BB * NN * 512 * 2);
+  u16* vxT   = (u16*)alloc((size_t)BB * 512 * NN * 2);
+  int* idxb  = (int*)alloc((size_t)BB * NN * 4);
   int* cnt   = (int*)alloc(64);
   float* lat = (float*)alloc((size_t)1024 * 1024 * 4);
-  u16* lnl   = (u16*)alloc((size_t)1024 * 1024 * 2);
-  u16* latn  = (u16*)alloc((size_t)1024 * 1024 * 2);
-  u16* qkv   = (u16*)alloc((size_t)1024 * 1536 * 2);
-  u16* aout  = (u16*)alloc((size_t)1024 * 512 * 2);
+  u16* qk    = (u16*)alloc((size_t)1024 * 1024 * 2);
+  u16* vlatT = (u16*)alloc((size_t)BB * 512 * 64 * 2);
   u16* hf    = (u16*)alloc((size_t)1024 * 4096 * 2);
   float* opart  = (float*)alloc((size_t)256 * 64 * 64 * 4);
   float* mlpart = (float*)alloc((size_t)256 * 128 * 4);
@@ -568,27 +786,26 @@
   u16* WoT   = (u16*)alloc((size_t)DEPTHC * 1024 * 512 * 2);
   u16* W1T   = (u16*)alloc((size_t)DEPTHC * 4096 * 1024 * 2);
   u16* W2T   = (u16*)alloc((size_t)DEPTHC * 1024 * 4096 * 2);
-  float* biaskv_all = (float*)alloc(DEPTHC * 1024 * 4);
-
-  maskscan_k<<<16, 256, 0, stream>>>(mask, idxb, cnt);
+  const int nbias = DEPTHC * (1536 + 1024 + 4096);
+  float* biasall = (float*)alloc((size_t)nbias * 4);
+
+  pre0_k<<<16 + 1024 + 40, 256, 0, stream>>>(mask, idxb, cnt, latents, lat, biasall, nbias);
   ln_gather_k<<<dim3(2048, 16), 256, 0, stream>>>(x, idxb, cnt, xcomp);
-  lat_init_k<<<1024, 256, 0, stream>>>(latents, lat);
-  zero_k<<<24, 256, 0, stream>>>(biaskv_all, DEPTHC * 1024);
-  transpall_k<<<DEPTHC * 10240, dim3(32, 8), 0, stream>>>(
-      Wq, Wkv, Wo, W1, W2, ln_m_w, ln_m_b,
-      WqkvT, WkvTf, WoT, W1T, W2T, biaskv_all);
+  transpall_k<<<DEPTHC * 2560, 256, 0, stream>>>(
+      Wq, Wkv, Wo, W1, W2, ln_l_w, ln_l_b, ln_m_w, ln_m_b, ff_ln_w, ff_ln_b,
+      WqkvT, WkvTf, WoT, W1T, W2T, biasall);
 
   for (int i = 0; i < DEPTHC; i++) {
-    ln_rows_k<false><<<1024, 256, 0, stream>>>(lat, ln_l_w + i*1024, ln_l_b + i*1024, lnl);
+    float* biasqkv = biasall + i * 1536;
+    float* biaskv  = biasall + DEPTHC*1536 + i * 1024;
+    float* bias1   = biasall + DEPTHC*1536 + DEPTHC*1024 + i * 4096;
     gemm_fused_k<<<2144, 256, 0, stream>>>(
-        xcomp, WkvTf + (size_t)i*1024*1024, kvx, biaskv_all + i*1024, cnt,
-        lnl, WqkvT + (size_t)i*1536*1024, qkv);
-    attn_part_k<<<256, 256, 0, stream>>>(qkv, kvx, cnt, opart, mlpart);
-    attn_comb_k<<<128, 256, 0, stream>>>(opart, mlpart, aout);
-    gemmsk_k<<<dim3(8, 8, 4), 256, 0, stream>>>(aout, WoT + (size_t)i*1024*512, lat, 1024, 1024, 512, 128);
-    ln_rows_k<false><<<1024, 256, 0, stream>>>(lat, ff_ln_w + i*1024, ff_ln_b + i*1024, latn);
-    gemm_gelu_k<<<dim3(32, 8), 256, 0, stream>>>(latn, W1T + (size_t)i*4096*1024, hf, 1024, 4096, 1024);
+        xcomp, WkvTf + (size_t)i*1024*1024, biaskv, kx, vxT, cnt,
+        lat, WqkvT + (size_t)i*1536*1024, biasqkv, qk, vlatT);
+    attn_part_k<<<256, 256, 0, stream>>>(qk, vlatT, kx, vxT, cnt, opart, mlpart);
+    gemm_wo_k<<<dim3(8, 8, 4), 256, 0, stream>>>(opart, mlpart, WoT + (size_t)i*1024*512, lat);
+    gemm_gelu_ln_k<<<dim3(32, 8), 256, 0, stream>>>(lat, W1T + (size_t)i*4096*1024, bias1, hf);
     gemmsk_k<<<dim3(8, 8, 4), 256, 0, stream>>>(hf, W2T + (size_t)i*1024*4096, lat, 1024, 1024, 4096, 1024);
   }
-  ln_rows_k<true><<<1024, 256, 0, stream>>>(lat, norm_w, norm_b, out);
-}
+  ln_final_k<<<1024, 256, 0, stream>>>(lat, norm_w, norm_b, out);
+}
```

New measurement: 1.967 ms. 31.4% more time.
